# Kernel optimization log

Hardware: AMD Instinct MI355X
Metric: run time of the kernel (lower is better)

Reference implementation:

```python
import jax, jax.numpy as jnp
import numpy as np

N_NODES = 20000
N_EDGES = 160000
EPS = 1e-5
LEAKY_SLOPE = 0.01


def gcn_conv(x, src, dst, W, b, num_nodes):
    """PyG GCNConv: self-loops + symmetric normalization. out = D^-1/2 A_hat D^-1/2 (x W) + b."""
    h = x @ W  # [N, out]
    loop = jnp.arange(num_nodes, dtype=src.dtype)
    s = jnp.concatenate([src, loop])
    d = jnp.concatenate([dst, loop])
    deg = jax.ops.segment_sum(jnp.ones_like(d, dtype=h.dtype), d, num_segments=num_nodes)
    dinv = jnp.where(deg > 0, jax.lax.rsqrt(jnp.maximum(deg, 1.0)) * jnp.where(deg > 0, 1.0, 0.0), 0.0)
    norm = dinv[s] * dinv[d]  # [E+N]
    msgs = h[s] * norm[:, None]  # gather + scale (memory-bound)
    out = jax.ops.segment_sum(msgs, d, num_segments=num_nodes)
    return out + b


def setup_inputs() -> dict:
    key = jax.random.key(0)
    ks = jax.random.split(key, 8)
    x = jax.random.normal(ks[0], (N_NODES, 1), dtype=jnp.float32)
    edge_index = jax.random.randint(ks[1], (2, N_EDGES), 0, N_NODES, dtype=jnp.int32)
    s = 0.02
    W1 = jax.random.normal(ks[2], (1, 2048), dtype=jnp.float32) * s
    b1 = jnp.zeros((2048,), jnp.float32)
    W2 = jax.random.normal(ks[3], (2048, 1024), dtype=jnp.float32) * s
    b2 = jnp.zeros((1024,), jnp.float32)
    gamma = jnp.ones((1024,), jnp.float32)
    beta = jnp.zeros((1024,), jnp.float32)
    running_mean = jnp.zeros((1024,), jnp.float32)
    running_var = jnp.ones((1024,), jnp.float32)
    lW1 = jax.random.normal(ks[4], (1024, 256), dtype=jnp.float32) * s
    lb1 = jnp.zeros((256,), jnp.float32)
    lW2 = jax.random.normal(ks[5], (256, 124), dtype=jnp.float32) * s
    lb2 = jnp.zeros((124,), jnp.float32)
    return dict(x=x, edge_index=edge_index, W1=W1, b1=b1, W2=W2, b2=b2,
                gamma=gamma, beta=beta, running_mean=running_mean,
                running_var=running_var, lW1=lW1, lb1=lb1, lW2=lW2, lb2=lb2)


def reference(x, edge_index, W1, b1, W2, b2, gamma, beta,
              running_mean, running_var, lW1, lb1, lW2, lb2):
    n = x.shape[0]
    src, dst = edge_index[0], edge_index[1]
    h = gcn_conv(x, src, dst, W1, b1, n)          # GCNConv(1, 2048); dropout is identity in eval
    h = gcn_conv(h, src, dst, W2, b2, n)          # GCNConv(2048, 1024)
    h = (h - running_mean) * (gamma * jax.lax.rsqrt(running_var + EPS)) + beta  # BatchNorm (eval)
    h = h @ lW1 + lb1                              # Linear 1024->256
    h = jnp.where(h >= 0, h, LEAKY_SLOPE * h)      # LeakyReLU
    h = h @ lW2 + lb2                              # Linear 256->124
    return jax.nn.log_softmax(h, axis=1)
```

## Files before the change

### kernel.cpp

```cpp
#include <hip/hip_runtime.h>
#include <math.h>

#define N_NODES 20000
#define N_EDGES 160000
#define EPSB 1e-5f
#define SLOPE 0.01f

typedef __attribute__((ext_vector_type(8))) short short8;
typedef __attribute__((ext_vector_type(4))) float f32x4;

#define OFF_DEG    0
#define OFF_AGG2   20000
#define OFF_V      40000
#define OFF_U      41024
#define OFF_R      42048
#define OFF_RU     42304
#define OFF_S      42560
#define OFF_ZEND   42816
#define OFF_DINV   42816
#define OFF_AGG1   62816
#define OFF_CNODE  82816
#define OFF_BFRAG  102816
#define OFF_RRS    119200

#define T_STRIDE 264

__device__ __forceinline__ unsigned short f2bf(float f) {
    unsigned u = __float_as_uint(f);
    return (unsigned short)((u + 0x7FFFu + ((u >> 16) & 1u)) >> 16);
}

__global__ void K1_deg_v(const int* __restrict__ dst, int* __restrict__ deg,
                         const float* __restrict__ W1, const float* __restrict__ b1,
                         const float* __restrict__ W2,
                         float* __restrict__ v, float* __restrict__ u) {
    int b = blockIdx.x;
    if (b < 625) {
        int e = b * 256 + threadIdx.x;
        atomicAdd(&deg[dst[e]], 1);
    } else {
        int bb = b - 625;
        int k  = (bb & 3) * 256 + threadIdx.x;
        int c0 = (bb >> 2) * 32;
        float av = 0.f, au = 0.f;
        for (int c = c0; c < c0 + 32; ++c) {
            float w = W2[c * 1024 + k];
            av = fmaf(W1[c], w, av);
            au = fmaf(b1[c], w, au);
        }
        atomicAdd(&v[k], av);
        atomicAdd(&u[k], au);
    }
}

__global__ void K2_prep_rs(const int* __restrict__ deg, const float* __restrict__ x,
                           float* __restrict__ dinv, float* __restrict__ agg1,
                           float* __restrict__ cnode,
                           const float* __restrict__ v, const float* __restrict__ u,
                           const float* __restrict__ gamma, const float* __restrict__ beta,
                           const float* __restrict__ mean, const float* __restrict__ var,
                           const float* __restrict__ b2, const float* __restrict__ lW1,
                           const float* __restrict__ lb1,
                           float* __restrict__ r, float* __restrict__ ru, float* __restrict__ s) {
    int b = blockIdx.x;
    if (b < 79) {
        int i = b * 256 + threadIdx.x;
        if (i < N_NODES) {
            float di = rsqrtf((float)(deg[i] + 1));
            dinv[i] = di;
            float d2 = di * di;
            agg1[i]  = d2 * x[i];
            cnode[i] = d2;
        }
    } else {
        int bb = b - 79, m = threadIdx.x, k0 = bb * 32;
        float ar = 0.f, aru = 0.f, as = 0.f;
        for (int k = k0; k < k0 + 32; ++k) {
            float g = gamma[k] * rsqrtf(var[k] + EPSB);
            float w = lW1[k * 256 + m];
            ar  = fmaf(v[k] * g, w, ar);
            aru = fmaf(u[k] * g, w, aru);
            as  = fmaf(fmaf(b2[k] - mean[k], g, beta[k]), w, as);
        }
        if (bb == 0) as += lb1[m];
        atomicAdd(&r[m], ar);
        atomicAdd(&ru[m], aru);
        atomicAdd(&s[m], as);
    }
}

__global__ void K3_edges1_bfrag(const int* __restrict__ src, const int* __restrict__ dst,
                                const float* __restrict__ dinv, const float* __restrict__ x,
                                float* __restrict__ agg1, float* __restrict__ cnode,
                                const float* __restrict__ lW2,
                                unsigned short* __restrict__ bfrag) {
    int b = blockIdx.x;
    if (b < 625) {
        int e = b * 256 + threadIdx.x;
        int sn = src[e], d = dst[e];
        float nrm = dinv[sn] * dinv[d];
        atomicAdd(&agg1[d], nrm * x[sn]);
        atomicAdd(&cnode[d], nrm);
    } else {
        int i = (b - 625) * 256 + threadIdx.x;
        int ct = i >> 9, ks = (i >> 6) & 7, lane = i & 63;
        int n  = ct * 16 + (lane & 15);
        int kb = ks * 32 + (lane >> 4) * 8;
        union { unsigned short u8[8]; short8 v8; } pk;
#pragma unroll
        for (int j = 0; j < 8; ++j)
            pk.u8[j] = (n < 124) ? f2bf(lW2[(kb + j) * 124 + n]) : (unsigned short)0;
        ((short8*)bfrag)[i] = pk.v8;
    }
}

__global__ void K4_edges2_rrs(const int* __restrict__ src, const int* __restrict__ dst,
                              const float* __restrict__ dinv, const float* __restrict__ agg1,
                              float* __restrict__ agg2,
                              const float* __restrict__ r, const float* __restrict__ ru,
                              const float* __restrict__ s, float4* __restrict__ rrs) {
    int b = blockIdx.x;
    if (b < 625) {
        int e = b * 256 + threadIdx.x;
        int sn = src[e], d = dst[e];
        atomicAdd(&agg2[d], dinv[sn] * dinv[d] * agg1[sn]);
    } else {
        int i = threadIdx.x;
        rrs[i] = make_float4(r[i], ru[i], s[i], 0.f);
    }
}

__global__ __launch_bounds__(256, 2) void KF_final(
    const float* __restrict__ agg2, const float* __restrict__ dinv,
    const float* __restrict__ agg1, const float* __restrict__ cnode,
    const float4* __restrict__ rrs, const short8* __restrict__ bfrag,
    const float* __restrict__ lb2, float* __restrict__ out) {
    __shared__ unsigned short tsh[16 * T_STRIDE];
    __shared__ float a_sh[16], cn_sh[16];
    __shared__ float logits[16 * 132];
    int tid  = threadIdx.x;
    int lane = tid & 63;
    int wave = __builtin_amdgcn_readfirstlane(tid >> 6);
    int row  = lane & 15, quad = lane >> 4;

    short8 bf0[8], bf1[8];
#pragma unroll
    for (int ks = 0; ks < 8; ++ks) {
        bf0[ks] = bfrag[((wave * 2 + 0) * 8 + ks) * 64 + lane];
        bf1[ks] = bfrag[((wave * 2 + 1) * 8 + ks) * 64 + lane];
    }
    float4 c = rrs[tid];

    for (int it = 0; it < 2; ++it) {
        int node0 = (blockIdx.x * 2 + it) * 16;
        if (tid < 16) {
            int n = node0 + tid;
            float di = dinv[n];
            a_sh[tid] = fmaf(di * di, agg1[n], agg2[n]);
        } else if (tid < 32) {
            cn_sh[tid - 16] = cnode[node0 + tid - 16];
        }
        __syncthreads();

#pragma unroll
        for (int n = 0; n < 16; ++n) {
            float t = fmaf(cn_sh[n], c.y, fmaf(a_sh[n], c.x, c.z));
            t = fmaf(SLOPE, fminf(t, 0.f), fmaxf(t, 0.f));
            tsh[n * T_STRIDE + tid] = f2bf(t);
        }
        __syncthreads();

        f32x4 acc0 = {0.f, 0.f, 0.f, 0.f}, acc1 = {0.f, 0.f, 0.f, 0.f};
        const unsigned short* tb = &tsh[row * T_STRIDE + quad * 8];
#pragma unroll
        for (int ks = 0; ks < 8; ++ks) {
            short8 af = *(const short8*)(tb + ks * 32);
            acc0 = __builtin_amdgcn_mfma_f32_16x16x32_bf16(af, bf0[ks], acc0, 0, 0, 0);
            acc1 = __builtin_amdgcn_mfma_f32_16x16x32_bf16(af, bf1[ks], acc1, 0, 0, 0);
        }
        int colbase = wave * 32;
#pragma unroll
        for (int rg = 0; rg < 4; ++rg) {
            int rw = quad * 4 + rg;
            logits[rw * 132 + colbase + row]      = acc0[rg];
            logits[rw * 132 + colbase + 16 + row] = acc1[rg];
        }
        __syncthreads();

        int nd = tid >> 4, sub = tid & 15, c0 = sub * 8;
        int jend = 124 - c0; if (jend > 8) jend = 8;
        float vbuf[8];
        const float* lrow = &logits[nd * 132 + c0];
        float mx = -1e30f;
        for (int j = 0; j < jend; ++j) {
            vbuf[j] = lrow[j] + lb2[c0 + j];
            mx = fmaxf(mx, vbuf[j]);
        }
        mx = fmaxf(mx, __shfl_xor(mx, 1, 16));
        mx = fmaxf(mx, __shfl_xor(mx, 2, 16));
        mx = fmaxf(mx, __shfl_xor(mx, 4, 16));
        mx = fmaxf(mx, __shfl_xor(mx, 8, 16));
        float sm = 0.f;
        for (int j = 0; j < jend; ++j) sm += __expf(vbuf[j] - mx);
        sm += __shfl_xor(sm, 1, 16);
        sm += __shfl_xor(sm, 2, 16);
        sm += __shfl_xor(sm, 4, 16);
        sm += __shfl_xor(sm, 8, 16);
        float lz = mx + __logf(sm);
        float* orow = out + (node0 + nd) * 124 + c0;
        for (int j = 0; j < jend; ++j) orow[j] = vbuf[j] - lz;
    }
}

extern "C" void kernel_launch(void* const* d_in, const int* in_sizes, int n_in,
                              void* d_out, int out_size, void* d_ws, size_t ws_size,
                              hipStream_t stream) {
    const float* x     = (const float*)d_in[0];
    const int*   ei    = (const int*)d_in[1];
    const int*   src   = ei;
    const int*   dst   = ei + N_EDGES;
    const float* W1    = (const float*)d_in[2];
    const float* b1    = (const float*)d_in[3];
    const float* W2    = (const float*)d_in[4];
    const float* b2    = (const float*)d_in[5];
    const float* gamma = (const float*)d_in[6];
    const float* beta  = (const float*)d_in[7];
    const float* rmean = (const float*)d_in[8];
    const float* rvar  = (const float*)d_in[9];
    const float* lW1   = (const float*)d_in[10];
    const float* lb1   = (const float*)d_in[11];
    const float* lW2   = (const float*)d_in[12];
    const float* lb2   = (const float*)d_in[13];
    float* out = (float*)d_out;
    float* ws  = (float*)d_ws;

    int*   deg   = (int*)(ws + OFF_DEG);
    float* agg2  = ws + OFF_AGG2;
    float* v     = ws + OFF_V;
    float* u     = ws + OFF_U;
    float* r     = ws + OFF_R;
    float* ru    = ws + OFF_RU;
    float* s     = ws + OFF_S;
    float* dinv  = ws + OFF_DINV;
    float* agg1  = ws + OFF_AGG1;
    float* cnode = ws + OFF_CNODE;
    unsigned short* bfrag = (unsigned short*)(ws + OFF_BFRAG);
    float4* rrs  = (float4*)(ws + OFF_RRS);

    hipMemsetAsync(ws, 0, OFF_ZEND * sizeof(float), stream);

    K1_deg_v<<<625 + 256, 256, 0, stream>>>(dst, deg, W1, b1, W2, v, u);
    K2_prep_rs<<<79 + 32, 256, 0, stream>>>(deg, x, dinv, agg1, cnode, v, u, gamma, beta,
                                            rmean, rvar, b2, lW1, lb1, r, ru, s);
    K3_edges1_bfrag<<<625 + 16, 256, 0, stream>>>(src, dst, dinv, x, agg1, cnode, lW2, bfrag);
    K4_edges2_rrs<<<625 + 1, 256, 0, stream>>>(src, dst, dinv, agg1, agg2, r, ru, s, rrs);
    KF_final<<<625, 256, 0, stream>>>(agg2, dinv, agg1, cnode, rrs,
                                      (const short8*)bfrag, lb2, out);
}
```

Before: 161.3 us.

## Remove dinv prep pass by computing degree normalization on the fly

Drops the separate node-prep kernel that stored dinv and initialized agg1/cnode. Each edge now computes its normalization directly from integer degrees, and self-loop terms are added later in the consumer kernels. The bfrag packing moves into the first kernel and the rrs packing kernel is removed, taking the launch count from five to four. In exchange, every edge recomputes rsqrt/reciprocal from two degree loads, and the memset now zeroes a larger region (a1, cn, a2).

```diff
diff --git a/kernel.cpp b/kernel.cpp
--- a/kernel.cpp
+++ b/kernel.cpp
@@ -10,18 +10,16 @@
 typedef __attribute__((ext_vector_type(4))) float f32x4;
 
 #define OFF_DEG    0
-#define OFF_AGG2   20000
-#define OFF_V      40000
-#define OFF_U      41024
-#define OFF_R      42048
-#define OFF_RU     42304
-#define OFF_S      42560
-#define OFF_ZEND   42816
-#define OFF_DINV   42816
-#define OFF_AGG1   62816
-#define OFF_CNODE  82816
-#define OFF_BFRAG  102816
-#define OFF_RRS    119200
+#define OFF_A1     20000
+#define OFF_CN     40000
+#define OFF_A2     60000
+#define OFF_V      80000
+#define OFF_U      81024
+#define OFF_R      82048
+#define OFF_RU     82304
+#define OFF_S      82560
+#define OFF_ZEND   82816
+#define OFF_BFRAG  82816
 
 #define T_STRIDE 264
 
@@ -30,15 +28,16 @@
     return (unsigned short)((u + 0x7FFFu + ((u >> 16) & 1u)) >> 16);
 }
 
-__global__ void K1_deg_v(const int* __restrict__ dst, int* __restrict__ deg,
-                         const float* __restrict__ W1, const float* __restrict__ b1,
-                         const float* __restrict__ W2,
-                         float* __restrict__ v, float* __restrict__ u) {
+__global__ void E1_deg_v_bf(const int* __restrict__ dst, int* __restrict__ deg,
+                            const float* __restrict__ W1, const float* __restrict__ b1,
+                            const float* __restrict__ W2, const float* __restrict__ lW2,
+                            float* __restrict__ v, float* __restrict__ u,
+                            unsigned short* __restrict__ bfrag) {
     int b = blockIdx.x;
     if (b < 625) {
         int e = b * 256 + threadIdx.x;
         atomicAdd(&deg[dst[e]], 1);
-    } else {
+    } else if (b < 881) {
         int bb = b - 625;
         int k  = (bb & 3) * 256 + threadIdx.x;
         int c0 = (bb >> 2) * 32;
@@ -50,30 +49,37 @@
         }
         atomicAdd(&v[k], av);
         atomicAdd(&u[k], au);
-    }
-}
-
-__global__ void K2_prep_rs(const int* __restrict__ deg, const float* __restrict__ x,
-                           float* __restrict__ dinv, float* __restrict__ agg1,
-                           float* __restrict__ cnode,
-                           const float* __restrict__ v, const float* __restrict__ u,
-                           const float* __restrict__ gamma, const float* __restrict__ beta,
-                           const float* __restrict__ mean, const float* __restrict__ var,
-                           const float* __restrict__ b2, const float* __restrict__ lW1,
-                           const float* __restrict__ lb1,
-                           float* __restrict__ r, float* __restrict__ ru, float* __restrict__ s) {
+    } else {
+        int i = (b - 881) * 256 + threadIdx.x;
+        int ct = i >> 9, ks = (i >> 6) & 7, lane = i & 63;
+        int n  = ct * 16 + (lane & 15);
+        int kb = ks * 32 + (lane >> 4) * 8;
+        union { unsigned short u8[8]; short8 v8; } pk;
+#pragma unroll
+        for (int j = 0; j < 8; ++j)
+            pk.u8[j] = (n < 124) ? f2bf(lW2[(kb + j) * 124 + n]) : (unsigned short)0;
+        ((short8*)bfrag)[i] = pk.v8;
+    }
+}
+
+__global__ void E2_edges1_rs(const int* __restrict__ src, const int* __restrict__ dst,
+                             const int* __restrict__ deg, const float* __restrict__ x,
+                             float* __restrict__ a1, float* __restrict__ cn,
+                             const float* __restrict__ v, const float* __restrict__ u,
+                             const float* __restrict__ gamma, const float* __restrict__ beta,
+                             const float* __restrict__ mean, const float* __restrict__ var,
+                             const float* __restrict__ b2, const float* __restrict__ lW1,
+                             const float* __restrict__ lb1,
+                             float* __restrict__ r, float* __restrict__ ru, float* __restrict__ s) {
     int b = blockIdx.x;
-    if (b < 79) {
-        int i = b * 256 + threadIdx.x;
-        if (i < N_NODES) {
-            float di = rsqrtf((float)(deg[i] + 1));
-            dinv[i] = di;
-            float d2 = di * di;
-            agg1[i]  = d2 * x[i];
-            cnode[i] = d2;
-        }
+    if (b < 625) {
+        int e = b * 256 + threadIdx.x;
+        int sn = src[e], d = dst[e];
+        float nrm = rsqrtf((float)((deg[sn] + 1) * (deg[d] + 1)));
+        atomicAdd(&a1[d], nrm * x[sn]);
+        atomicAdd(&cn[d], nrm);
     } else {
-        int bb = b - 79, m = threadIdx.x, k0 = bb * 32;
+        int bb = b - 625, m = threadIdx.x, k0 = bb * 32;
         float ar = 0.f, aru = 0.f, as = 0.f;
         for (int k = k0; k < k0 + 32; ++k) {
             float g = gamma[k] * rsqrtf(var[k] + EPSB);
@@ -89,52 +95,25 @@
     }
 }
 
-__global__ void K3_edges1_bfrag(const int* __restrict__ src, const int* __restrict__ dst,
-                                const float* __restrict__ dinv, const float* __restrict__ x,
-                                float* __restrict__ agg1, float* __restrict__ cnode,
-                                const float* __restrict__ lW2,
-                                unsigned short* __restrict__ bfrag) {
-    int b = blockIdx.x;
-    if (b < 625) {
-        int e = b * 256 + threadIdx.x;
-        int sn = src[e], d = dst[e];
-        float nrm = dinv[sn] * dinv[d];
-        atomicAdd(&agg1[d], nrm * x[sn]);
-        atomicAdd(&cnode[d], nrm);
-    } else {
-        int i = (b - 625) * 256 + threadIdx.x;
-        int ct = i >> 9, ks = (i >> 6) & 7, lane = i & 63;
-        int n  = ct * 16 + (lane & 15);
-        int kb = ks * 32 + (lane >> 4) * 8;
-        union { unsigned short u8[8]; short8 v8; } pk;
-#pragma unroll
-        for (int j = 0; j < 8; ++j)
-            pk.u8[j] = (n < 124) ? f2bf(lW2[(kb + j) * 124 + n]) : (unsigned short)0;
-        ((short8*)bfrag)[i] = pk.v8;
-    }
-}
-
-__global__ void K4_edges2_rrs(const int* __restrict__ src, const int* __restrict__ dst,
-                              const float* __restrict__ dinv, const float* __restrict__ agg1,
-                              float* __restrict__ agg2,
-                              const float* __restrict__ r, const float* __restrict__ ru,
-                              const float* __restrict__ s, float4* __restrict__ rrs) {
-    int b = blockIdx.x;
-    if (b < 625) {
-        int e = b * 256 + threadIdx.x;
-        int sn = src[e], d = dst[e];
-        atomicAdd(&agg2[d], dinv[sn] * dinv[d] * agg1[sn]);
-    } else {
-        int i = threadIdx.x;
-        rrs[i] = make_float4(r[i], ru[i], s[i], 0.f);
-    }
-}
-
-__global__ __launch_bounds__(256, 2) void KF_final(
-    const float* __restrict__ agg2, const float* __restrict__ dinv,
-    const float* __restrict__ agg1, const float* __restrict__ cnode,
-    const float4* __restrict__ rrs, const short8* __restrict__ bfrag,
-    const float* __restrict__ lb2, float* __restrict__ out) {
+__global__ void E3_edges2(const int* __restrict__ src, const int* __restrict__ dst,
+                          const int* __restrict__ deg, const float* __restrict__ x,
+                          const float* __restrict__ a1, float* __restrict__ a2) {
+    int e = blockIdx.x * 256 + threadIdx.x;
+    int sn = src[e], d = dst[e];
+    float i_s = 1.f / (float)(deg[sn] + 1);
+    float dd  = rsqrtf((float)(deg[d] + 1));
+    float a1f = fmaf(i_s, x[sn], a1[sn]);
+    atomicAdd(&a2[d], sqrtf(i_s) * dd * a1f);
+}
+
+__global__ __launch_bounds__(256, 2) void F_final(
+    const int* __restrict__ deg, const float* __restrict__ x,
+    const float* __restrict__ a1, const float* __restrict__ cn,
+    const float* __restrict__ a2,
+    const float* __restrict__ r, const float* __restrict__ ru,
+    const float* __restrict__ s,
+    const short8* __restrict__ bfrag, const float* __restrict__ lb2,
+    float* __restrict__ out) {
     __shared__ unsigned short tsh[16 * T_STRIDE];
     __shared__ float a_sh[16], cn_sh[16];
     __shared__ float logits[16 * 132];
@@ -149,22 +128,22 @@
         bf0[ks] = bfrag[((wave * 2 + 0) * 8 + ks) * 64 + lane];
         bf1[ks] = bfrag[((wave * 2 + 1) * 8 + ks) * 64 + lane];
     }
-    float4 c = rrs[tid];
+    float cr = r[tid], cu = ru[tid], cs = s[tid];
 
     for (int it = 0; it < 2; ++it) {
         int node0 = (blockIdx.x * 2 + it) * 16;
         if (tid < 16) {
             int n = node0 + tid;
-            float di = dinv[n];
-            a_sh[tid] = fmaf(di * di, agg1[n], agg2[n]);
-        } else if (tid < 32) {
-            cn_sh[tid - 16] = cnode[node0 + tid - 16];
+            float d2  = 1.f / (float)(deg[n] + 1);
+            float a1f = fmaf(d2, x[n], a1[n]);
+            a_sh[tid]  = fmaf(d2, a1f, a2[n]);
+            cn_sh[tid] = cn[n] + d2;
         }
         __syncthreads();
 
 #pragma unroll
         for (int n = 0; n < 16; ++n) {
-            float t = fmaf(cn_sh[n], c.y, fmaf(a_sh[n], c.x, c.z));
+            float t = fmaf(cn_sh[n], cu, fmaf(a_sh[n], cr, cs));
             t = fmaf(SLOPE, fminf(t, 0.f), fmaxf(t, 0.f));
             tsh[n * T_STRIDE + tid] = f2bf(t);
         }
@@ -234,26 +213,23 @@
     float* out = (float*)d_out;
     float* ws  = (float*)d_ws;
 
-    int*   deg   = (int*)(ws + OFF_DEG);
-    float* agg2  = ws + OFF_AGG2;
-    float* v     = ws + OFF_V;
-    float* u     = ws + OFF_U;
-    float* r     = ws + OFF_R;
-    float* ru    = ws + OFF_RU;
-    float* s     = ws + OFF_S;
-    float* dinv  = ws + OFF_DINV;
-    float* agg1  = ws + OFF_AGG1;
-    float* cnode = ws + OFF_CNODE;
+    int*   deg = (int*)(ws + OFF_DEG);
+    float* a1  = ws + OFF_A1;
+    float* cn  = ws + OFF_CN;
+    float* a2  = ws + OFF_A2;
+    float* v   = ws + OFF_V;
+    float* u   = ws + OFF_U;
+    float* r   = ws + OFF_R;
+    float* ru  = ws + OFF_RU;
+    float* s   = ws + OFF_S;
     unsigned short* bfrag = (unsigned short*)(ws + OFF_BFRAG);
-    float4* rrs  = (float4*)(ws + OFF_RRS);
 
     hipMemsetAsync(ws, 0, OFF_ZEND * sizeof(float), stream);
 
-    K1_deg_v<<<625 + 256, 256, 0, stream>>>(dst, deg, W1, b1, W2, v, u);
-    K2_prep_rs<<<79 + 32, 256, 0, stream>>>(deg, x, dinv, agg1, cnode, v, u, gamma, beta,
-                                            rmean, rvar, b2, lW1, lb1, r, ru, s);
-    K3_edges1_bfrag<<<625 + 16, 256, 0, stream>>>(src, dst, dinv, x, agg1, cnode, lW2, bfrag);
-    K4_edges2_rrs<<<625 + 1, 256, 0, stream>>>(src, dst, dinv, agg1, agg2, r, ru, s, rrs);
-    KF_final<<<625, 256, 0, stream>>>(agg2, dinv, agg1, cnode, rrs,
-                                      (const short8*)bfrag, lb2, out);
-}
+    E1_deg_v_bf<<<625 + 256 + 16, 256, 0, stream>>>(dst, deg, W1, b1, W2, lW2, v, u, bfrag);
+    E2_edges1_rs<<<625 + 32, 256, 0, stream>>>(src, dst, deg, x, a1, cn, v, u, gamma, beta,
+                                               rmean, rvar, b2, lW1, lb1, r, ru, s);
+    E3_edges2<<<625, 256, 0, stream>>>(src, dst, deg, x, a1, a2);
+    F_final<<<625, 256, 0, stream>>>(deg, x, a1, cn, a2, r, ru, s,
+                                     (const short8*)bfrag, lb2, out);
+}
```

New measurement: 150.9 us. 1.07x faster.
